# Performance work log

Hardware: AMD Instinct MI355X
Metric: run time of the kernel (lower is better)

## Reference

```python
import jax, jax.numpy as jnp
import numpy as np

B, M, DM = 8, 1024, 1024
H, DH, R = 16, 64, 32
DFF, R1, R2, RO = 4096, 512, 512, 512
EPS = 1e-12


def layernorm(x, g, b):
    mu = jnp.mean(x, axis=-1, keepdims=True)
    var = jnp.mean(jnp.square(x - mu), axis=-1, keepdims=True)
    return (x - mu) * jax.lax.rsqrt(var + EPS) * g + b


def setup_inputs() -> dict:
    key = jax.random.key(0)
    ks = jax.random.split(key, 24)
    s = lambda *sh: 1.0 / np.sqrt(sh[-2] if len(sh) > 1 else sh[-1])
    d = {}
    d['x'] = jax.random.normal(ks[0], (B, M, DM), jnp.float32)
    d['mask'] = jnp.zeros((B, M), jnp.float32)  # additive attention mask
    # per-head low-rank QKV factors: P:(H,DM,R), V:(H,R,DH), b:(H,DH)
    for i, nm in enumerate(['q', 'k', 'v']):
        d['P' + nm] = jax.random.normal(ks[1 + 3 * i], (H, DM, R), jnp.float32) * 0.02
        d['V' + nm] = jax.random.normal(ks[2 + 3 * i], (H, R, DH), jnp.float32) * 0.02
        d['b' + nm] = jnp.zeros((H, DH), jnp.float32)
    # attention output projection (low-rank) + LN1
    d['Uo'] = jax.random.normal(ks[10], (DM, RO), jnp.float32) * 0.02
    d['Vo'] = jax.random.normal(ks[11], (RO, DM), jnp.float32) * 0.02
    d['bo_attn'] = jnp.zeros((DM,), jnp.float32)
    d['g1'] = jnp.ones((DM,), jnp.float32)
    d['beta1'] = jnp.zeros((DM,), jnp.float32)
    # FFN low-rank factors + LN2
    d['U1'] = jax.random.normal(ks[12], (DM, R1), jnp.float32) * 0.02
    d['V1'] = jax.random.normal(ks[13], (R1, DFF), jnp.float32) * 0.02
    d['b1'] = jnp.zeros((DFF,), jnp.float32)
    d['U2'] = jax.random.normal(ks[14], (DFF, R2), jnp.float32) * 0.02
    d['V2'] = jax.random.normal(ks[15], (R2, DM), jnp.float32) * 0.02
    d['b2'] = jnp.zeros((DM,), jnp.float32)
    d['g2'] = jnp.ones((DM,), jnp.float32)
    d['beta2'] = jnp.zeros((DM,), jnp.float32)
    return d


def reference(x, mask, Pq, Vq, bq, Pk, Vk, bk, Pv, Vv, bv,
              Uo, Vo, bo_attn, g1, beta1,
              U1, V1, b1, U2, V2, b2, g2, beta2):
    # low-rank Q/K/V: x @ P -> (B,H,M,R), then @ V -> (B,H,M,DH), + bias
    def qkv(P, V, b):
        tmp = jnp.einsum('bmd,hdr->bhmr', x, P)
        return jnp.einsum('bhmr,hre->bhme', tmp, V) + b[None, :, None, :]

    Q = qkv(Pq, Vq, bq)
    K = qkv(Pk, Vk, bk)
    V = qkv(Pv, Vv, bv)
    scale = 1.0 / jnp.sqrt(jnp.asarray(DH, x.dtype))
    scores = jnp.einsum('bhme,bhne->bhmn', Q, K) * scale
    scores = scores + mask[:, None, None, :]  # additive mask broadcast over heads/queries
    probs = jax.nn.softmax(scores, axis=-1)
    attn = jnp.einsum('bhmn,bhne->bhme', probs, V)  # (B,H,M,DH)
    attn = attn.transpose(0, 2, 1, 3).reshape(attn.shape[0], attn.shape[2], -1)  # (B,M,DM)
    x1 = layernorm(x + (attn @ Uo) @ Vo + bo_attn, g1, beta1)
    # FFN: GELU((x1 @ U1) @ V1 + b1) @ U2 @ V2 + b2 (flashsvd_ffn semantics)
    mid = x1 @ U1
    hidden = jax.nn.gelu(mid @ V1 + b1, approximate=False)
    y = (hidden @ U2) @ V2 + b2
    return layernorm(x1 + y, g2, beta2)
```

## Files before the change

kernel.cpp:

```cpp
#include <hip/hip_runtime.h>
#include <hip/hip_bf16.h>
#include <math.h>

typedef unsigned short u16;
typedef unsigned int u32;
typedef __attribute__((ext_vector_type(8))) short bf16x8;
typedef __attribute__((ext_vector_type(4))) float f32x4;
typedef __attribute__((ext_vector_type(2))) unsigned int u32x2;
typedef __attribute__((ext_vector_type(4))) unsigned int u32x4;

#define B_ 8
#define M_ 1024
#define DM_ 1024
#define H_ 16
#define DH_ 64
#define NR_ 8192

__device__ __forceinline__ u16 f2bf(float f) {
    unsigned u = __float_as_uint(f);
    u += 0x7FFFu + ((u >> 16) & 1u);
    return (u16)(u >> 16);
}

__device__ __forceinline__ void gload16(const void* g, void* l) {
    __builtin_amdgcn_global_load_lds(
        (const __attribute__((address_space(1))) void*)g,
        (__attribute__((address_space(3))) void*)l, 16, 0, 0);
}

__device__ __forceinline__ u32 lds_addr(const void* p) {
    return (u32)(uintptr_t)(const __attribute__((address_space(3))) void*)p;
}

__device__ void conv_dev(const float* __restrict__ in, u16* __restrict__ out,
                         int bid, int tid) {
#pragma unroll
    for (int j = 0; j < 4; ++j) {
        int i = bid * 4096 + j * 1024 + tid * 4;
        float4 v = *reinterpret_cast<const float4*>(in + i);
        unsigned long long p = (unsigned long long)f2bf(v.x)
                             | ((unsigned long long)f2bf(v.y) << 16)
                             | ((unsigned long long)f2bf(v.z) << 32)
                             | ((unsigned long long)f2bf(v.w) << 48);
        *reinterpret_cast<unsigned long long*>(out + i) = p;
    }
}

__device__ void prep_p_dev(const float* __restrict__ P, u16* __restrict__ Pt,
                           int h, int kc, int tid, float* sm) {
    float (*Ps)[33] = (float(*)[33])sm;
#pragma unroll
    for (int i = 0; i < 16; ++i) {
        int e = tid + i * 256;
        int kk = e >> 5, r = e & 31;
        Ps[kk][r] = P[(size_t)h * 32768 + (size_t)(kc + kk) * 32 + r];
    }
    __syncthreads();
#pragma unroll
    for (int i = 0; i < 16; ++i) {
        int e = tid + i * 256;
        int r = e >> 7, k = e & 127;
        Pt[(size_t)(h * 32 + r) * 1024 + kc + k] = f2bf(Ps[k][r]);
    }
}

__device__ void prep_f_dev(const float* __restrict__ V, u16* __restrict__ Ft,
                           int h, int tid, float* sm) {
    float (*Vs)[65] = (float(*)[65])sm;
#pragma unroll
    for (int i = 0; i < 8; ++i) {
        int e = tid + i * 256;
        int r = e >> 6, c = e & 63;
        Vs[r][c] = V[(size_t)h * 2048 + r * 64 + c];
    }
    __syncthreads();
#pragma unroll
    for (int i = 0; i < 8; ++i) {
        int idx = tid + i * 256;
        int e = idx >> 5, r = idx & 31;
        Ft[(size_t)h * 2560 + e * 40 + r] = f2bf(Vs[r][e]);
    }
}

__device__ void transp_dev(const float* __restrict__ in, u16* __restrict__ out,
                           int R, int C, int bx, int by, int tid, float* sm) {
    float (*t)[65] = (float(*)[65])sm;
    const int rb = by * 64, cb = bx * 64;
#pragma unroll
    for (int i = 0; i < 16; ++i) {
        int e = tid + i * 256;
        int r = e >> 6, c = e & 63;
        t[r][c] = in[(size_t)(rb + r) * C + cb + c];
    }
    __syncthreads();
#pragma unroll
    for (int i = 0; i < 16; ++i) {
        int e = tid + i * 256;
        int r = e >> 6, c = e & 63;
        out[(size_t)(cb + r) * R + rb + c] = f2bf(t[c][r]);
    }
}

__global__ __launch_bounds__(256) void prep_all(
    const float* __restrict__ x,
    const float* __restrict__ Pq, const float* __restrict__ Pk, const float* __restrict__ Pv,
    const float* __restrict__ Vq, const float* __restrict__ Vk, const float* __restrict__ Vv,
    const float* __restrict__ Uo, const float* __restrict__ Vo,
    const float* __restrict__ U1, const float* __restrict__ V1,
    const float* __restrict__ U2, const float* __restrict__ V2,
    u16* __restrict__ Xb, u16* __restrict__ Pt,
    u16* __restrict__ Ftq, u16* __restrict__ Ftk, u16* __restrict__ Ftv,
    u16* __restrict__ Uot, u16* __restrict__ Vot,
    u16* __restrict__ U1t, u16* __restrict__ V1t,
    u16* __restrict__ U2t, u16* __restrict__ V2t) {
    __shared__ float smem[4224];
    const int bid = blockIdx.x, tid = threadIdx.x;
    if (bid < 2048) {
        conv_dev(x, Xb, bid, tid);
    } else if (bid < 2432) {
        int t = bid - 2048, which = t >> 7, tt = t & 127;
        const float* P = which == 0 ? Pq : (which == 1 ? Pk : Pv);
        prep_p_dev(P, Pt + (size_t)which * 524288, tt >> 3, (tt & 7) * 128, tid, smem);
    } else if (bid < 2480) {
        int t = bid - 2432, which = t >> 4;
        const float* V = which == 0 ? Vq : (which == 1 ? Vk : Vv);
        u16* F = which == 0 ? Ftq : (which == 1 ? Ftk : Ftv);
        prep_f_dev(V, F, t & 15, tid, smem);
    } else if (bid < 2608) {
        int t = bid - 2480;
        transp_dev(Uo, Uot, 1024, 512, t & 7, t >> 3, tid, smem);
    } else if (bid < 2736) {
        int t = bid - 2608;
        transp_dev(Vo, Vot, 512, 1024, t & 15, t >> 4, tid, smem);
    } else if (bid < 2864) {
        int t = bid - 2736;
        transp_dev(U1, U1t, 1024, 512, t & 7, t >> 3, tid, smem);
    } else if (bid < 3376) {
        int t = bid - 2864;
        transp_dev(V1, V1t, 512, 4096, t & 63, t >> 6, tid, smem);
    } else if (bid < 3888) {
        int t = bid - 3376;
        transp_dev(U2, U2t, 4096, 512, t & 7, t >> 3, tid, smem);
    } else {
        int t = bid - 3888;
        transp_dev(V2, V2t, 512, 1024, t & 15, t >> 4, tid, smem);
    }
}

template <int EPI, int NF>
__global__ __launch_bounds__(256) void gemm_bf16(const u16* __restrict__ A,
                                                 const u16* __restrict__ Bt,
                                                 const float* __restrict__ bias,
                                                 void* __restrict__ Cout,
                                                 int K, int N) {
    constexpr int BN = NF * 32;
    __shared__ u16 As[128 * 64];
    __shared__ u16 Bs[BN * 64];
    const int tid = threadIdx.x;
    const int lane = tid & 63, wv = tid >> 6;

    const int NX = gridDim.x;
    const int flat = blockIdx.x + blockIdx.y * NX;
    const int q = (NX * gridDim.y) >> 3;
    const int nid = (flat & 7) * q + (flat >> 3);
    const int row0 = (nid / NX) * 128, col0 = (nid % NX) * BN;

    const int frow = lane & 15, fk8 = lane >> 4;
    const int wm = (wv >> 1) * 64, wn = (wv & 1) * (BN / 2);

    f32x4 acc[4][NF];
    const f32x4 z4 = {0.f, 0.f, 0.f, 0.f};
#pragma unroll
    for (int i = 0; i < 4; ++i)
#pragma unroll
        for (int j = 0; j < NF; ++j) acc[i][j] = z4;

    for (int k0 = 0; k0 < K; k0 += 64) {
#pragma unroll
        for (int i = 0; i < 4; ++i) {
            int rr = (i * 4 + wv) * 8 + (lane >> 3);
            int cc = ((lane & 7) ^ (rr & 7)) * 8;
            gload16(A + (size_t)(row0 + rr) * K + k0 + cc,
                    (char*)As + (i * 4 + wv) * 1024);
        }
#pragma unroll
        for (int i = 0; i < NF; ++i) {
            int rr = (i * 4 + wv) * 8 + (lane >> 3);
            int cc = ((lane & 7) ^ (rr & 7)) * 8;
            gload16(Bt + (size_t)(col0 + rr) * K + k0 + cc,
                    (char*)Bs + (i * 4 + wv) * 1024);
        }
        asm volatile("s_waitcnt vmcnt(0)" ::: "memory");
        __syncthreads();
#pragma unroll
        for (int kf = 0; kf < 2; ++kf) {
            bf16x8 af[4], bfr[NF];
#pragma unroll
            for (int mf = 0; mf < 4; ++mf) {
                int r = wm + mf * 16 + frow;
                int c16 = (kf * 4 + fk8) ^ (r & 7);
                af[mf] = *reinterpret_cast<const bf16x8*>((char*)As + r * 128 + c16 * 16);
            }
#pragma unroll
            for (int nf = 0; nf < NF; ++nf) {
                int r = wn + nf * 16 + frow;
                int c16 = (kf * 4 + fk8) ^ (r & 7);
                bfr[nf] = *reinterpret_cast<const bf16x8*>((char*)Bs + r * 128 + c16 * 16);
            }
#pragma unroll
            for (int mf = 0; mf < 4; ++mf)
#pragma unroll
                for (int nf = 0; nf < NF; ++nf)
                    acc[mf][nf] = __builtin_amdgcn_mfma_f32_16x16x32_bf16(
                        af[mf], bfr[nf], acc[mf][nf], 0, 0, 0);
        }
        __syncthreads();
    }

    const int orow = fk8 * 4, ocol = frow;
#pragma unroll
    for (int mf = 0; mf < 4; ++mf)
#pragma unroll
        for (int nf = 0; nf < NF; ++nf)
#pragma unroll
            for (int j = 0; j < 4; ++j) {
                int row = row0 + wm + mf * 16 + orow + j;
                int col = col0 + wn + nf * 16 + ocol;
                float v = acc[mf][nf][j];
                if (EPI == 2) {
                    v += bias[col];
                    v = 0.5f * v * (1.f + erff(v * 0.70710678118f));
                    ((u16*)Cout)[(size_t)row * N + col] = f2bf(v);
                } else if (EPI == 3) {
                    ((float*)Cout)[(size_t)row * N + col] = v;
                } else {
                    ((u16*)Cout)[(size_t)row * N + col] = f2bf(v);
                }
            }
}

__global__ __launch_bounds__(256) void gemm_qkv(const u16* __restrict__ A,
                                                const u16* __restrict__ Bt,
                                                const u16* __restrict__ Ftq,
                                                const u16* __restrict__ Ftk,
                                                const u16* __restrict__ Ftv,
                                                const float* __restrict__ bq,
                                                const float* __restrict__ bk,
                                                const float* __restrict__ bv,
                                                u16* __restrict__ Qo,
                                                u16* __restrict__ Ko,
                                                u16* __restrict__ Vo) {
    const int K = 1024;
    __shared__ u16 As[128 * 64];
    __shared__ u16 Bs[128 * 64];
    const int tid = threadIdx.x;
    const int lane = tid & 63, wv = tid >> 6;

    const int NX = gridDim.x;
    const int flat = blockIdx.x + blockIdx.y * NX;
    const int q = (NX * gridDim.y) >> 3;
    const int nid = (flat & 7) * q + (flat >> 3);
    const int row0 = (nid / NX) * 128, col0 = (nid % NX) * 128;

    const int frow = lane & 15, fk8 = lane >> 4;
    const int wm = (wv >> 1) * 64, wn = (wv & 1) * 64;

    f32x4 acc[4][4];
    const f32x4 z4 = {0.f, 0.f, 0.f, 0.f};
#pragma unroll
    for (int i = 0; i < 4; ++i)
#pragma unroll
        for (int j = 0; j < 4; ++j) acc[i][j] = z4;

    for (int k0 = 0; k0 < K; k0 += 64) {
#pragma unroll
        for (int i = 0; i < 4; ++i) {
            int rr = (i * 4 + wv) * 8 + (lane >> 3);
            int cc = ((lane & 7) ^ (rr & 7)) * 8;
            gload16(A + (size_t)(row0 + rr) * K + k0 + cc,
                    (char*)As + (i * 4 + wv) * 1024);
            gload16(Bt + (size_t)(col0 + rr) * K + k0 + cc,
                    (char*)Bs + (i * 4 + wv) * 1024);
        }
        asm volatile("s_waitcnt vmcnt(0)" ::: "memory");
        __syncthreads();
#pragma unroll
        for (int kf = 0; kf < 2; ++kf) {
            bf16x8 af[4], bfr[4];
#pragma unroll
            for (int mf = 0; mf < 4; ++mf) {
                int r = wm + mf * 16 + frow;
                int c16 = (kf * 4 + fk8) ^ (r & 7);
                af[mf] = *reinterpret_cast<const bf16x8*>((char*)As + r * 128 + c16 * 16);
            }
#pragma unroll
            for (int nf = 0; nf < 4; ++nf) {
                int r = wn + nf * 16 + frow;
                int c16 = (kf * 4 + fk8) ^ (r & 7);
                bfr[nf] = *reinterpret_cast<const bf16x8*>((char*)Bs + r * 128 + c16 * 16);
            }
#pragma unroll
            for (int mf = 0; mf < 4; ++mf)
#pragma unroll
                for (int nf = 0; nf < 4; ++nf)
                    acc[mf][nf] = __builtin_amdgcn_mfma_f32_16x16x32_bf16(
                        af[mf], bfr[nf], acc[mf][nf], 0, 0, 0);
        }
        __syncthreads();
    }

    u16* preg = (wv < 2) ? As + wv * 4096 : Bs + (wv - 2) * 4096;
#pragma unroll
    for (int mf = 0; mf < 4; ++mf)
#pragma unroll
        for (int nf = 0; nf < 4; ++nf)
#pragma unroll
            for (int j = 0; j < 4; ++j) {
                int r = mf * 16 + fk8 * 4 + j;
                int c = nf * 16 + frow;
                int byte = r * 128 + (((c >> 3) ^ (r & 7)) * 16) + (c & 7) * 2;
                *(u16*)((char*)preg + byte) = f2bf(acc[mf][nf][j]);
            }
    __syncthreads();

    const int f = col0 >> 9;
    const u16* Ft = f == 0 ? Ftq : (f == 1 ? Ftk : Ftv);
    const float* bias = f == 0 ? bq : (f == 1 ? bk : bv);
    u16* outp = f == 0 ? Qo : (f == 1 ? Ko : Vo);
    const int h0 = (((col0 & 511) + wn) >> 5);

#pragma unroll
    for (int hh = 0; hh < 2; ++hh) {
        const int h = h0 + hh;
        const u16* ftb = Ft + (size_t)h * 2560;
        bf16x8 bf2[4];
#pragma unroll
        for (int ef = 0; ef < 4; ++ef) {
            int e = ef * 16 + frow;
            bf2[ef] = *reinterpret_cast<const bf16x8*>(ftb + e * 40 + fk8 * 8);
        }
#pragma unroll
        for (int mf = 0; mf < 4; ++mf) {
            int r = mf * 16 + frow;
            bf16x8 af = *reinterpret_cast<const bf16x8*>(
                (char*)preg + r * 128 + (((hh * 4 + fk8) ^ (r & 7)) * 16));
#pragma unroll
            for (int ef = 0; ef < 4; ++ef) {
                f32x4 o = __builtin_amdgcn_mfma_f32_16x16x32_bf16(af, bf2[ef], z4, 0, 0, 0);
                int e = ef * 16 + frow;
                float bv_ = bias[h * 64 + e];
#pragma unroll
                for (int j = 0; j < 4; ++j) {
                    int row = row0 + wm + mf * 16 + fk8 * 4 + j;
                    int bb = row >> 10, m = row & 1023;
                    outp[(((size_t)(bb * 16 + h) << 10) + m) * 64 + e] = f2bf(o[j] + bv_);
                }
            }
        }
    }
}

__global__ __launch_bounds__(256) void gemm_db(const u16* __restrict__ A,
                                               const u16* __restrict__ Bt,
                                               u16* __restrict__ Cout,
                                               int K, int N) {
    __shared__ u16 As[2][128 * 64];
    __shared__ u16 Bs[2][64 * 64];
    const int tid = threadIdx.x;
    const int lane = tid & 63, wv = tid >> 6;

    const int NX = gridDim.x;
    const int flat = blockIdx.x + blockIdx.y * NX;
    const int q = (NX * gridDim.y) >> 3;
    const int nid = (flat & 7) * q + (flat >> 3);
    const int row0 = (nid / NX) * 128, col0 = (nid % NX) * 64;

    const int frow = lane & 15, fk8 = lane >> 4;
    const int wm = (wv >> 1) * 64, wn = (wv & 1) * 32;

    f32x4 acc[4][2];
    const f32x4 z4 = {0.f, 0.f, 0.f, 0.f};
#pragma unroll
    for (int i = 0; i < 4; ++i) {
        acc[i][0] = z4;
        acc[i][1] = z4;
    }

    const int srr = (lane >> 3);
    const int scc = (lane & 7);

#pragma unroll
    for (int i = 0; i < 4; ++i) {
        int rr = (i * 4 + wv) * 8 + srr;
        int cc = (scc ^ (rr & 7)) * 8;
        gload16(A + (size_t)(row0 + rr) * K + cc, (char*)&As[0][0] + (i * 4 + wv) * 1024);
    }
#pragma unroll
    for (int i = 0; i < 2; ++i) {
        int rr = (i * 4 + wv) * 8 + srr;
        int cc = (scc ^ (rr & 7)) * 8;
        gload16(Bt + (size_t)(col0 + rr) * K + cc, (char*)&Bs[0][0] + (i * 4 + wv) * 1024);
    }

    int cur = 0;
    for (int k0 = 0; k0 < K; k0 += 64) {
        __syncthreads();
        if (k0 + 64 < K) {
            int kn = k0 + 64;
#pragma unroll
            for (int i = 0; i < 4; ++i) {
                int rr = (i * 4 + wv) * 8 + srr;
                int cc = (scc ^ (rr & 7)) * 8;
                gload16(A + (size_t)(row0 + rr) * K + kn + cc,
                        (char*)&As[cur ^ 1][0] + (i * 4 + wv) * 1024);
            }
#pragma unroll
            for (int i = 0; i < 2; ++i) {
                int rr = (i * 4 + wv) * 8 + srr;
                int cc = (scc ^ (rr & 7)) * 8;
                gload16(Bt + (size_t)(col0 + rr) * K + kn + cc,
                        (char*)&Bs[cur ^ 1][0] + (i * 4 + wv) * 1024);
            }
        }
#pragma unroll
        for (int kf = 0; kf < 2; ++kf) {
            bf16x8 af[4], bfr[2];
#pragma unroll
            for (int mf = 0; mf < 4; ++mf) {
                int r = wm + mf * 16 + frow;
                int c16 = (kf * 4 + fk8) ^ (r & 7);
                af[mf] = *reinterpret_cast<const bf16x8*>((char*)&As[cur][0] + r * 128 + c16 * 16);
            }
#pragma unroll
            for (int nf = 0; nf < 2; ++nf) {
                int r = wn + nf * 16 + frow;
                int c16 = (kf * 4 + fk8) ^ (r & 7);
                bfr[nf] = *reinterpret_cast<const bf16x8*>((char*)&Bs[cur][0] + r * 128 + c16 * 16);
            }
#pragma unroll
            for (int mf = 0; mf < 4; ++mf)
#pragma unroll
                for (int nf = 0; nf < 2; ++nf)
                    acc[mf][nf] = __builtin_amdgcn_mfma_f32_16x16x32_bf16(
                        af[mf], bfr[nf], acc[mf][nf], 0, 0, 0);
        }
        cur ^= 1;
    }

#pragma unroll
    for (int mf = 0; mf < 4; ++mf)
#pragma unroll
        for (int nf = 0; nf < 2; ++nf)
#pragma unroll
            for (int j = 0; j < 4; ++j) {
                int row = row0 + wm + mf * 16 + fk8 * 4 + j;
                int col = col0 + wn + nf * 16 + frow;
                Cout[(size_t)row * N + col] = f2bf(acc[mf][nf][j]);
            }
}

__global__ __launch_bounds__(256, 8) void attn_mfma(const u16* __restrict__ Q,
                                                    const u16* __restrict__ K,
                                                    const u16* __restrict__ V,
                                                    const float* __restrict__ mask,
                                                    u16* __restrict__ O) {
    __shared__ u16 Ks[4096];
    __shared__ u16 Vt[8448];
    const int flat = blockIdx.x;
    const int nid = (flat & 7) * 256 + (flat >> 3);
    const int hb = nid >> 4, qt = nid & 15;
    const int b = hb >> 4, h = hb & 15;
    const int tid = threadIdx.x, lane = tid & 63, wv = tid >> 6;
    const int frow = lane & 15, fk8 = lane >> 4;
    const size_t base = (size_t)hb * 65536;
    const float LOG2E = 1.44269504089f;
    const int srr = lane >> 3, scc = lane & 7;

    int voff[2];
#pragma unroll
    for (int i = 0; i < 2; ++i) {
        int r = i * 4 + wv;
        int keyp = (2 * (r >> 2) + (lane >> 5)) * 16 + (r & 3) * 4 + ((lane >> 1) & 3);
        int d = ((lane >> 3) & 3) * 16 + (lane & 1) * 8;
        voff[i] = keyp * 64 + d;
    }

#pragma unroll
    for (int i = 0; i < 2; ++i) {
        int rr = (i * 4 + wv) * 8 + srr;
        int cc = (scc ^ (rr & 7)) * 8;
        gload16(Q + base + (size_t)(qt * 64 + rr) * 64 + cc,
                (char*)Vt + (i * 4 + wv) * 1024);
    }
    asm volatile("s_waitcnt vmcnt(0)" ::: "memory");
    __syncthreads();
    bf16x8 qfrag[2];
#pragma unroll
    for (int kf = 0; kf < 2; ++kf) {
        int qr = wv * 16 + frow;
        int c16 = (kf * 4 + fk8) ^ (qr & 7);
        qfrag[kf] = *reinterpret_cast<const bf16x8*>((char*)Vt + qr * 128 + c16 * 16);
    }
    __syncthreads();
#pragma unroll
    for (int i = 0; i < 2; ++i) {
        int rr = (i * 4 + wv) * 8 + srr;
        int cc = (scc ^ (rr & 7)) * 8;
        gload16(K + base + (size_t)rr * 64 + cc, (char*)Ks + (i * 4 + wv) * 1024);
    }
#pragma unroll
    for (int i = 0; i < 2; ++i)
        gload16(V + base + voff[i], (char*)Vt + (i * 4 + wv) * 1056);
    asm volatile("s_waitcnt vmcnt(0)" ::: "memory");
    __syncthreads();

    const u32 plbase = lds_addr(Vt) + fk8 * 1056 + frow * 2;
    const float* mrow = mask + b * M_;

    float m_i = -1e30f, l_i = 0.f;
    const f32x4 z4 = {0.f, 0.f, 0.f, 0.f};
    f32x4 o_acc[4] = {z4, z4, z4, z4};

    int cur = 0;
    for (int kt = 0; kt < 16; ++kt) {
        f32x4 sacc[4] = {z4, z4, z4, z4};
        __builtin_amdgcn_s_setprio(1);
#pragma unroll
        for (int kf = 0; kf < 2; ++kf)
#pragma unroll
            for (int nf = 0; nf < 4; ++nf) {
                int kr = nf * 16 + frow;
                int c16 = (kf * 4 + fk8) ^ (kr & 7);
                bf16x8 ak = *reinterpret_cast<const bf16x8*>((char*)Ks + kr * 128 + c16 * 16);
                sacc[nf] = __builtin_amdgcn_mfma_f32_16x16x32_bf16(ak, qfrag[kf], sacc[nf], 0, 0, 0);
            }
        __builtin_amdgcn_s_setprio(0);
        __syncthreads();

        if (kt < 15) {
            const int nxt = cur ^ 1;
#pragma unroll
            for (int i = 0; i < 2; ++i) {
                int rr = (i * 4 + wv) * 8 + srr;
                int cc = (scc ^ (rr & 7)) * 8;
                gload16(K + base + (kt + 1) * 4096 + (size_t)rr * 64 + cc,
                        (char*)Ks + (i * 4 + wv) * 1024);
            }
#pragma unroll
            for (int i = 0; i < 2; ++i)
                gload16(V + base + (kt + 1) * 4096 + voff[i],
                        (char*)Vt + nxt * 8448 + (i * 4 + wv) * 1056);
        }

        float tval[4][4];
        float tmax = -1e30f;
#pragma unroll
        for (int nf = 0; nf < 4; ++nf) {
            float4 mk = *reinterpret_cast<const float4*>(mrow + kt * 64 + nf * 16 + fk8 * 4);
            float t0 = fmaf(sacc[nf][0], 0.125f, mk.x);
            float t1 = fmaf(sacc[nf][1], 0.125f, mk.y);
            float t2 = fmaf(sacc[nf][2], 0.125f, mk.z);
            float t3 = fmaf(sacc[nf][3], 0.125f, mk.w);
            tval[nf][0] = t0; tval[nf][1] = t1; tval[nf][2] = t2; tval[nf][3] = t3;
            tmax = fmaxf(tmax, fmaxf(fmaxf(t0, t1), fmaxf(t2, t3)));
        }
        tmax = fmaxf(tmax, __shfl_xor(tmax, 16));
        tmax = fmaxf(tmax, __shfl_xor(tmax, 32));

        if (__any(tmax > m_i + 8.f)) {
            float mnew = fmaxf(m_i, tmax);
            float c = exp2f((m_i - mnew) * LOG2E);
            m_i = mnew;
            l_i *= c;
#pragma unroll
            for (int j = 0; j < 4; ++j) {
                float cj = __shfl(c, fk8 * 4 + j);
#pragma unroll
                for (int nf = 0; nf < 4; ++nf) o_acc[nf][j] *= cj;
            }
        }

        const float ml = m_i * LOG2E;
        float rs = 0.f;
        u32 w0[4], w1[4];
#pragma unroll
        for (int nf = 0; nf < 4; ++nf) {
            float p0 = exp2f(fmaf(tval[nf][0], LOG2E, -ml));
            float p1 = exp2f(fmaf(tval[nf][1], LOG2E, -ml));
            float p2 = exp2f(fmaf(tval[nf][2], LOG2E, -ml));
            float p3 = exp2f(fmaf(tval[nf][3], LOG2E, -ml));
            rs += (p0 + p1) + (p2 + p3);
            w0[nf] = __builtin_amdgcn_perm(__float_as_uint(p1), __float_as_uint(p0), 0x07060302u);
            w1[nf] = __builtin_amdgcn_perm(__float_as_uint(p3), __float_as_uint(p2), 0x07060302u);
        }
        rs += __shfl_xor(rs, 16);
        rs += __shfl_xor(rs, 32);
        l_i += rs;

        const u32 vb = plbase + (u32)(cur * 8448);
#pragma unroll
        for (int kf = 0; kf < 2; ++kf) {
            u32x4 apv = {w0[kf * 2], w1[kf * 2], w0[kf * 2 + 1], w1[kf * 2 + 1]};
            bf16x8 ap;
            __builtin_memcpy(&ap, &apv, 16);
            u32 a = vb + (u32)(kf * 4224);
            u32x2 r0, r1, r2, r3, r4, r5, r6, r7;
            asm volatile("ds_read_b64_tr_b16 %0, %1" : "=&v"(r0) : "v"(a));
            asm volatile("ds_read_b64_tr_b16 %0, %1 offset:512" : "=&v"(r1) : "v"(a));
            asm volatile("ds_read_b64_tr_b16 %0, %1 offset:128" : "=&v"(r2) : "v"(a));
            asm volatile("ds_read_b64_tr_b16 %0, %1 offset:640" : "=&v"(r3) : "v"(a));
            asm volatile("ds_read_b64_tr_b16 %0, %1 offset:256" : "=&v"(r4) : "v"(a));
            asm volatile("ds_read_b64_tr_b16 %0, %1 offset:768" : "=&v"(r5) : "v"(a));
            asm volatile("ds_read_b64_tr_b16 %0, %1 offset:384" : "=&v"(r6) : "v"(a));
            asm volatile("ds_read_b64_tr_b16 %0, %1 offset:896" : "=&v"(r7) : "v"(a));
            asm volatile("s_waitcnt lgkmcnt(0)" ::: "memory");
            __builtin_amdgcn_sched_barrier(0);
            __builtin_amdgcn_s_setprio(1);
            {
                u32x4 vv = {r0.x, r0.y, r1.x, r1.y};
                bf16x8 fb; __builtin_memcpy(&fb, &vv, 16);
                o_acc[0] = __builtin_amdgcn_mfma_f32_16x16x32_bf16(ap, fb, o_acc[0], 0, 0, 0);
            }
            {
                u32x4 vv = {r2.x, r2.y, r3.x, r3.y};
                bf16x8 fb; __builtin_memcpy(&fb, &vv, 16);
                o_acc[1] = __builtin_amdgcn_mfma_f32_16x16x32_bf16(ap, fb, o_acc[1], 0, 0, 0);
            }
            {
                u32x4 vv = {r4.x, r4.y, r5.x, r5.y};
                bf16x8 fb; __builtin_memcpy(&fb, &vv, 16);
                o_acc[2] = __builtin_amdgcn_mfma_f32_16x16x32_bf16(ap, fb, o_acc[2], 0, 0, 0);
            }
            {
                u32x4 vv = {r6.x, r6.y, r7.x, r7.y};
                bf16x8 fb; __builtin_memcpy(&fb, &vv, 16);
                o_acc[3] = __builtin_amdgcn_mfma_f32_16x16x32_bf16(ap, fb, o_acc[3], 0, 0, 0);
            }
            __builtin_amdgcn_s_setprio(0);
        }

        asm volatile("s_waitcnt vmcnt(0)" ::: "memory");
        __syncthreads();
        cur ^= 1;
    }

#pragma unroll
    for (int j = 0; j < 4; ++j) {
        float lq = __shfl(l_i, fk8 * 4 + j);
        float inv = 1.f / lq;
        int grow = qt * 64 + wv * 16 + fk8 * 4 + j;
        size_t obase = ((size_t)(b * M_ + grow)) * DM_ + h * 64;
#pragma unroll
        for (int nf = 0; nf < 4; ++nf)
            O[obase + nf * 16 + frow] = f2bf(o_acc[nf][j] * inv);
    }
}

template <bool WBF>
__global__ __launch_bounds__(256) void ln_kernel(const float* __restrict__ y,
                                                 const float* __restrict__ res,
                                                 const float* __restrict__ bias,
                                                 const float* __restrict__ g,
                                                 const float* __restrict__ beta,
                                                 float* __restrict__ outf,
                                                 u16* __restrict__ outb) {
    __shared__ float red[2][4];
    const int row = blockIdx.x, tid = threadIdx.x;
    const size_t base = (size_t)row * 1024 + tid * 4;
    float4 v = *reinterpret_cast<const float4*>(y + base);
    float4 r = *reinterpret_cast<const float4*>(res + base);
    float4 bb = *reinterpret_cast<const float4*>(bias + tid * 4);
    v.x += r.x + bb.x; v.y += r.y + bb.y; v.z += r.z + bb.z; v.w += r.w + bb.w;
    float sum = v.x + v.y + v.z + v.w;
    float sq = v.x * v.x + v.y * v.y + v.z * v.z + v.w * v.w;
#pragma unroll
    for (int off = 32; off; off >>= 1) {
        sum += __shfl_down(sum, off);
        sq += __shfl_down(sq, off);
    }
    if ((tid & 63) == 0) { red[0][tid >> 6] = sum; red[1][tid >> 6] = sq; }
    __syncthreads();
    sum = red[0][0] + red[0][1] + red[0][2] + red[0][3];
    sq = red[1][0] + red[1][1] + red[1][2] + red[1][3];
    float mu = sum * (1.f / 1024.f);
    float var = sq * (1.f / 1024.f) - mu * mu;
    float rstd = rsqrtf(var + 1e-12f);
    float4 gg = *reinterpret_cast<const float4*>(g + tid * 4);
    float4 be = *reinterpret_cast<const float4*>(beta + tid * 4);
    float4 o;
    o.x = (v.x - mu) * rstd * gg.x + be.x;
    o.y = (v.y - mu) * rstd * gg.y + be.y;
    o.z = (v.z - mu) * rstd * gg.z + be.z;
    o.w = (v.w - mu) * rstd * gg.w + be.w;
    *reinterpret_cast<float4*>(outf + base) = o;
    if (WBF) {
        unsigned long long p = (unsigned long long)f2bf(o.x)
                             | ((unsigned long long)f2bf(o.y) << 16)
                             | ((unsigned long long)f2bf(o.z) << 32)
                             | ((unsigned long long)f2bf(o.w) << 48);
        *reinterpret_cast<unsigned long long*>(outb + base) = p;
    }
}

extern "C" void kernel_launch(void* const* d_in, const int* in_sizes, int n_in,
                              void* d_out, int out_size, void* d_ws, size_t ws_size,
                              hipStream_t stream) {
    const float* x    = (const float*)d_in[0];
    const float* mask = (const float*)d_in[1];
    const float* Pq   = (const float*)d_in[2];
    const float* Vq   = (const float*)d_in[3];
    const float* bq   = (const float*)d_in[4];
    const float* Pk   = (const float*)d_in[5];
    const float* Vk   = (const float*)d_in[6];
    const float* bk   = (const float*)d_in[7];
    const float* Pv   = (const float*)d_in[8];
    const float* Vv   = (const float*)d_in[9];
    const float* bv   = (const float*)d_in[10];
    const float* Uo   = (const float*)d_in[11];
    const float* Vo   = (const float*)d_in[12];
    const float* bo   = (const float*)d_in[13];
    const float* g1   = (const float*)d_in[14];
    const float* be1  = (const float*)d_in[15];
    const float* U1   = (const float*)d_in[16];
    const float* V1   = (const float*)d_in[17];
    const float* b1   = (const float*)d_in[18];
    const float* U2   = (const float*)d_in[19];
    const float* V2   = (const float*)d_in[20];
    const float* b2   = (const float*)d_in[21];
    const float* g2   = (const float*)d_in[22];
    const float* be2  = (const float*)d_in[23];
    float* out = (float*)d_out;

    const size_t MB = 1048576;
    char* ws = (char*)d_ws;
    u16* Pt  = (u16*)(ws + 0);
    u16* Ftq = (u16*)(ws + 3 * MB);
    u16* Ftk = (u16*)(ws + 3 * MB + 131072);
    u16* Ftv = (u16*)(ws + 3 * MB + 262144);
    u16* Uot = (u16*)(ws + 4 * MB);
    u16* Vot = (u16*)(ws + 5 * MB);
    u16* U1t = (u16*)(ws + 6 * MB);
    u16* V1t = (u16*)(ws + 7 * MB);
    u16* U2t = (u16*)(ws + 11 * MB);
    u16* V2t = (u16*)(ws + 15 * MB);
    u16* Xb  = (u16*)(ws + 16 * MB);
    u16* Qb  = (u16*)(ws + 56 * MB);
    u16* Kb  = (u16*)(ws + 72 * MB);
    u16* Vb  = (u16*)(ws + 88 * MB);
    u16* Ob  = (u16*)(ws + 104 * MB);
    u16* Hb  = (u16*)(ws + 32 * MB);
    float* Yf = (float*)(ws + 56 * MB);
    u16* Tb  = (u16*)(ws + 96 * MB);
    float* X1f = (float*)(ws + 120 * MB);

    prep_all<<<4016, 256, 0, stream>>>(x, Pq, Pk, Pv, Vq, Vk, Vv,
                                       Uo, Vo, U1, V1, U2, V2,
                                       Xb, Pt, Ftq, Ftk, Ftv,
                                       Uot, Vot, U1t, V1t, U2t, V2t);

    gemm_qkv<<<dim3(12, 64), 256, 0, stream>>>(Xb, Pt, Ftq, Ftk, Ftv,
                                               bq, bk, bv, Qb, Kb, Vb);

    attn_mfma<<<2048, 256, 0, stream>>>(Qb, Kb, Vb, mask, Ob);

    gemm_db<<<dim3(8, 64), 256, 0, stream>>>(Ob, Uot, Tb, 1024, 512);
    gemm_bf16<3, 4><<<dim3(8, 64), 256, 0, stream>>>(Tb, Vot, nullptr, Yf, 512, 1024);
    ln_kernel<true><<<8192, 256, 0, stream>>>(Yf, x, bo, g1, be1, X1f, Xb);

    gemm_db<<<dim3(8, 64), 256, 0, stream>>>(Xb, U1t, Tb, 1024, 512);
    gemm_bf16<2, 4><<<dim3(32, 64), 256, 0, stream>>>(Tb, V1t, b1, Hb, 512, 4096);
    gemm_db<<<dim3(8, 64), 256, 0, stream>>>(Hb, U2t, Tb, 4096, 512);
    gemm_bf16<3, 4><<<dim3(8, 64), 256, 0, stream>>>(Tb, V2t, nullptr, Yf, 512, 1024);
    ln_kernel<false><<<8192, 256, 0, stream>>>(Yf, X1f, b2, g2, be2, out, nullptr);
}
```

Before: 338.8 us.

## Use bf16 intermediates for LN inputs and enlarge attention blocks to 128 queries

The projection GEMMs now write bf16 instead of fp32 outputs, and the layernorm kernels read bf16 inputs. The second layernorm takes its residual from the bf16 copy of x1 rather than an fp32 copy, which removes the fp32 X1 buffer and cuts memory traffic. Attention blocks grow to 512 threads covering 128 queries each, so every K/V tile load is shared by twice as many query rows. Q fragments are now loaded straight from global memory instead of staged through LDS. The bf16 residual and outputs lower precision, and using more threads per block may change occupancy.

```diff
diff --git a/kernel.cpp b/kernel.cpp
--- a/kernel.cpp
+++ b/kernel.cpp
@@ -20,6 +20,10 @@
     unsigned u = __float_as_uint(f);
     u += 0x7FFFu + ((u >> 16) & 1u);
     return (u16)(u >> 16);
+}
+
+__device__ __forceinline__ float bf2f(u16 v) {
+    return __uint_as_float((u32)v << 16);
 }
 
 __device__ __forceinline__ void gload16(const void* g, void* l) {
@@ -231,8 +235,6 @@
                     v += bias[col];
                     v = 0.5f * v * (1.f + erff(v * 0.70710678118f));
                     ((u16*)Cout)[(size_t)row * N + col] = f2bf(v);
-                } else if (EPI == 3) {
-                    ((float*)Cout)[(size_t)row * N + col] = v;
                 } else {
                     ((u16*)Cout)[(size_t)row * N + col] = f2bf(v);
                 }
@@ -459,7 +461,7 @@
             }
 }
 
-__global__ __launch_bounds__(256, 8) void attn_mfma(const u16* __restrict__ Q,
+__global__ __launch_bounds__(512, 8) void attn_mfma(const u16* __restrict__ Q,
                                                     const u16* __restrict__ K,
                                                     const u16* __restrict__ V,
                                                     const float* __restrict__ mask,
@@ -467,50 +469,34 @@
     __shared__ u16 Ks[4096];
     __shared__ u16 Vt[8448];
     const int flat = blockIdx.x;
-    const int nid = (flat & 7) * 256 + (flat >> 3);
-    const int hb = nid >> 4, qt = nid & 15;
+    const int nid = (flat & 7) * 128 + (flat >> 3);
+    const int hb = nid >> 3, qt = nid & 7;
     const int b = hb >> 4, h = hb & 15;
     const int tid = threadIdx.x, lane = tid & 63, wv = tid >> 6;
     const int frow = lane & 15, fk8 = lane >> 4;
     const size_t base = (size_t)hb * 65536;
     const float LOG2E = 1.44269504089f;
-    const int srr = lane >> 3, scc = lane & 7;
-
-    int voff[2];
-#pragma unroll
-    for (int i = 0; i < 2; ++i) {
-        int r = i * 4 + wv;
+
+    const int krr = wv * 8 + (lane >> 3);
+    const int kcc = ((lane & 7) ^ (krr & 7)) * 8;
+
+    int voff;
+    {
+        int r = wv;
         int keyp = (2 * (r >> 2) + (lane >> 5)) * 16 + (r & 3) * 4 + ((lane >> 1) & 3);
         int d = ((lane >> 3) & 3) * 16 + (lane & 1) * 8;
-        voff[i] = keyp * 64 + d;
-    }
-
-#pragma unroll
-    for (int i = 0; i < 2; ++i) {
-        int rr = (i * 4 + wv) * 8 + srr;
-        int cc = (scc ^ (rr & 7)) * 8;
-        gload16(Q + base + (size_t)(qt * 64 + rr) * 64 + cc,
-                (char*)Vt + (i * 4 + wv) * 1024);
-    }
-    asm volatile("s_waitcnt vmcnt(0)" ::: "memory");
-    __syncthreads();
+        voff = keyp * 64 + d;
+    }
+
     bf16x8 qfrag[2];
-#pragma unroll
-    for (int kf = 0; kf < 2; ++kf) {
-        int qr = wv * 16 + frow;
-        int c16 = (kf * 4 + fk8) ^ (qr & 7);
-        qfrag[kf] = *reinterpret_cast<const bf16x8*>((char*)Vt + qr * 128 + c16 * 16);
-    }
-    __syncthreads();
-#pragma unroll
-    for (int i = 0; i < 2; ++i) {
-        int rr = (i * 4 + wv) * 8 + srr;
-        int cc = (scc ^ (rr & 7)) * 8;
-        gload16(K + base + (size_t)rr * 64 + cc, (char*)Ks + (i * 4 + wv) * 1024);
-    }
-#pragma unroll
-    for (int i = 0; i < 2; ++i)
-        gload16(V + base + voff[i], (char*)Vt + (i * 4 + wv) * 1056);
+    {
+        const u16* qrow = Q + base + (size_t)(qt * 128 + wv * 16 + frow) * 64;
+        qfrag[0] = *reinterpret_cast<const bf16x8*>(qrow + fk8 * 8);
+        qfrag[1] = *reinterpret_cast<const bf16x8*>(qrow + 32 + fk8 * 8);
+    }
+
+    gload16(K + base + (size_t)krr * 64 + kcc, (char*)Ks + wv * 1024);
+    gload16(V + base + voff, (char*)Vt + wv * 1056);
     asm volatile("s_waitcnt vmcnt(0)" ::: "memory");
     __syncthreads();
 
@@ -539,17 +525,10 @@
 
         if (kt < 15) {
             const int nxt = cur ^ 1;
-#pragma unroll
-            for (int i = 0; i < 2; ++i) {
-                int rr = (i * 4 + wv) * 8 + srr;
-                int cc = (scc ^ (rr & 7)) * 8;
-                gload16(K + base + (kt + 1) * 4096 + (size_t)rr * 64 + cc,
-                        (char*)Ks + (i * 4 + wv) * 1024);
-            }
-#pragma unroll
-            for (int i = 0; i < 2; ++i)
-                gload16(V + base + (kt + 1) * 4096 + voff[i],
-                        (char*)Vt + nxt * 8448 + (i * 4 + wv) * 1056);
+            gload16(K + base + (kt + 1) * 4096 + (size_t)krr * 64 + kcc,
+                    (char*)Ks + wv * 1024);
+            gload16(V + base + (kt + 1) * 4096 + voff,
+                    (char*)Vt + nxt * 8448 + wv * 1056);
         }
 
         float tval[4][4];
@@ -648,7 +627,7 @@
     for (int j = 0; j < 4; ++j) {
         float lq = __shfl(l_i, fk8 * 4 + j);
         float inv = 1.f / lq;
-        int grow = qt * 64 + wv * 16 + fk8 * 4 + j;
+        int grow = qt * 128 + wv * 16 + fk8 * 4 + j;
         size_t obase = ((size_t)(b * M_ + grow)) * DM_ + h * 64;
 #pragma unroll
         for (int nf = 0; nf < 4; ++nf)
@@ -656,23 +635,37 @@
     }
 }
 
-template <bool WBF>
-__global__ __launch_bounds__(256) void ln_kernel(const float* __restrict__ y,
-                                                 const float* __restrict__ res,
-                                                 const float* __restrict__ bias,
-                                                 const float* __restrict__ g,
-                                                 const float* __restrict__ beta,
-                                                 float* __restrict__ outf,
-                                                 u16* __restrict__ outb) {
+template <int MODE>
+__global__ __launch_bounds__(256) void ln_bf(const u16* __restrict__ y,
+                                             const float* __restrict__ resf,
+                                             const u16* __restrict__ resb,
+                                             const float* __restrict__ bias,
+                                             const float* __restrict__ g,
+                                             const float* __restrict__ beta,
+                                             float* __restrict__ outf,
+                                             u16* __restrict__ outb) {
     __shared__ float red[2][4];
     const int row = blockIdx.x, tid = threadIdx.x;
     const size_t base = (size_t)row * 1024 + tid * 4;
-    float4 v = *reinterpret_cast<const float4*>(y + base);
-    float4 r = *reinterpret_cast<const float4*>(res + base);
+
+    u32x2 yp = *reinterpret_cast<const u32x2*>(y + base);
+    float v0 = bf2f((u16)(yp.x & 0xFFFF)), v1 = bf2f((u16)(yp.x >> 16));
+    float v2 = bf2f((u16)(yp.y & 0xFFFF)), v3 = bf2f((u16)(yp.y >> 16));
+
+    float r0, r1, r2, r3;
+    if (MODE == 0) {
+        float4 r = *reinterpret_cast<const float4*>(resf + base);
+        r0 = r.x; r1 = r.y; r2 = r.z; r3 = r.w;
+    } else {
+        u32x2 rp = *reinterpret_cast<const u32x2*>(resb + base);
+        r0 = bf2f((u16)(rp.x & 0xFFFF)); r1 = bf2f((u16)(rp.x >> 16));
+        r2 = bf2f((u16)(rp.y & 0xFFFF)); r3 = bf2f((u16)(rp.y >> 16));
+    }
     float4 bb = *reinterpret_cast<const float4*>(bias + tid * 4);
-    v.x += r.x + bb.x; v.y += r.y + bb.y; v.z += r.z + bb.z; v.w += r.w + bb.w;
-    float sum = v.x + v.y + v.z + v.w;
-    float sq = v.x * v.x + v.y * v.y + v.z * v.z + v.w * v.w;
+    v0 += r0 + bb.x; v1 += r1 + bb.y; v2 += r2 + bb.z; v3 += r3 + bb.w;
+
+    float sum = v0 + v1 + v2 + v3;
+    float sq = v0 * v0 + v1 * v1 + v2 * v2 + v3 * v3;
 #pragma unroll
     for (int off = 32; off; off >>= 1) {
         sum += __shfl_down(sum, off);
@@ -687,17 +680,18 @@
     float rstd = rsqrtf(var + 1e-12f);
     float4 gg = *reinterpret_cast<const float4*>(g + tid * 4);
     float4 be = *reinterpret_cast<const float4*>(beta + tid * 4);
-    float4 o;
-    o.x = (v.x - mu) * rstd * gg.x + be.x;
-    o.y = (v.y - mu) * rstd * gg.y + be.y;
-    o.z = (v.z - mu) * rstd * gg.z + be.z;
-    o.w = (v.w - mu) * rstd * gg.w + be.w;
-    *reinterpret_cast<float4*>(outf + base) = o;
-    if (WBF) {
-        unsigned long long p = (unsigned long long)f2bf(o.x)
-                             | ((unsigned long long)f2bf(o.y) << 16)
-                             | ((unsigned long long)f2bf(o.z) << 32)
-                             | ((unsigned long long)f2bf(o.w) << 48);
+    float o0 = (v0 - mu) * rstd * gg.x + be.x;
+    float o1 = (v1 - mu) * rstd * gg.y + be.y;
+    float o2 = (v2 - mu) * rstd * gg.z + be.z;
+    float o3 = (v3 - mu) * rstd * gg.w + be.w;
+    if (MODE == 1) {
+        float4 o = {o0, o1, o2, o3};
+        *reinterpret_cast<float4*>(outf + base) = o;
+    } else {
+        unsigned long long p = (unsigned long long)f2bf(o0)
+                             | ((unsigned long long)f2bf(o1) << 16)
+                             | ((unsigned long long)f2bf(o2) << 32)
+                             | ((unsigned long long)f2bf(o3) << 48);
         *reinterpret_cast<unsigned long long*>(outb + base) = p;
     }
 }
@@ -749,9 +743,8 @@
     u16* Vb  = (u16*)(ws + 88 * MB);
     u16* Ob  = (u16*)(ws + 104 * MB);
     u16* Hb  = (u16*)(ws + 32 * MB);
-    float* Yf = (float*)(ws + 56 * MB);
+    u16* Yb  = (u16*)(ws + 56 * MB);
     u16* Tb  = (u16*)(ws + 96 * MB);
-    float* X1f = (float*)(ws + 120 * MB);
 
     prep_all<<<4016, 256, 0, stream>>>(x, Pq, Pk, Pv, Vq, Vk, Vv,
                                        Uo, Vo, U1, V1, U2, V2,
@@ -761,15 +754,15 @@
     gemm_qkv<<<dim3(12, 64), 256, 0, stream>>>(Xb, Pt, Ftq, Ftk, Ftv,
                                                bq, bk, bv, Qb, Kb, Vb);
 
-    attn_mfma<<<2048, 256, 0, stream>>>(Qb, Kb, Vb, mask, Ob);
+    attn_mfma<<<1024, 512, 0, stream>>>(Qb, Kb, Vb, mask, Ob);
 
     gemm_db<<<dim3(8, 64), 256, 0, stream>>>(Ob, Uot, Tb, 1024, 512);
-    gemm_bf16<3, 4><<<dim3(8, 64), 256, 0, stream>>>(Tb, Vot, nullptr, Yf, 512, 1024);
-    ln_kernel<true><<<8192, 256, 0, stream>>>(Yf, x, bo, g1, be1, X1f, Xb);
+    gemm_bf16<0, 4><<<dim3(8, 64), 256, 0, stream>>>(Tb, Vot, nullptr, Yb, 512, 1024);
+    ln_bf<0><<<8192, 256, 0, stream>>>(Yb, x, nullptr, bo, g1, be1, nullptr, Xb);
 
     gemm_db<<<dim3(8, 64), 256, 0, stream>>>(Xb, U1t, Tb, 1024, 512);
     gemm_bf16<2, 4><<<dim3(32, 64), 256, 0, stream>>>(Tb, V1t, b1, Hb, 512, 4096);
     gemm_db<<<dim3(8, 64), 256, 0, stream>>>(Hb, U2t, Tb, 4096, 512);
-    gemm_bf16<3, 4><<<dim3(8, 64), 256, 0, stream>>>(Tb, V2t, nullptr, Yf, 512, 1024);
-    ln_kernel<false><<<8192, 256, 0, stream>>>(Yf, X1f, b2, g2, be2, out, nullptr);
-}
+    gemm_bf16<0, 4><<<dim3(8, 64), 256, 0, stream>>>(Tb, V2t, nullptr, Yb, 512, 1024);
+    ln_bf<1><<<8192, 256, 0, stream>>>(Yb, nullptr, Xb, b2, g2, be2, out, nullptr);
+}
```

Measured after the change: 331.5 us. 2.2% less time.
